# Kernel optimization log

Measured on AMD Instinct MI355X. Metric: run time of the kernel, lower is better.

## Reference

```python
import jax, jax.numpy as jnp
import numpy as np

# static config (mirrors init_kwargs)
B, IMG_C, IN_C, OUT_C, S = 16, 3, 256, 512, 128
HIDDEN = IN_C                     # min(out_dim, in_dim) in DepthwiseSynthesisKernel
KGEN_IN = 32                      # (3+1)//2 * 4 * (512//128)
KSIZE = 3                         # generated depthwise kernel taps (= conv_kernel)
NUM_TAPS = KGEN_IN - 2 * KSIZE + 2  # 28, low-pass filter taps
CUTOFF, HALFWIDTH = 32.0, 7.35
CONV_CLAMP = 256.0
LRELU_GAIN = float(np.sqrt(2.0))  # bias_act def_gain for lrelu
DN = ('NCHW', 'OIHW', 'NCHW')

def _firwin(numtaps, cutoff, width, fs):
    # numpy re-implementation of scipy.signal.firwin (kaiser window, lowpass)
    nyq = fs / 2.0
    atten = 2.285 * (numtaps - 1) * np.pi * (width / nyq) + 7.95
    if atten > 50:
        beta = 0.1102 * (atten - 8.7)
    elif atten > 21:
        beta = 0.5842 * (atten - 21) ** 0.4 + 0.07886 * (atten - 21)
    else:
        beta = 0.0
    m = np.arange(numtaps) - (numtaps - 1) / 2.0
    c = cutoff / nyq
    h = c * np.sinc(c * m) * np.kaiser(numtaps, beta)
    return (h / h.sum()).astype(np.float32)

def setup_inputs():
    key = jax.random.key(0)
    ks = jax.random.split(key, 9)
    img = jax.random.normal(ks[0], (B, IMG_C, S, S), jnp.float32)
    fromrgb_w = jax.random.normal(ks[1], (IN_C, IMG_C, 1, 1), jnp.float32)
    fromrgb_b = jnp.zeros((IN_C,), jnp.float32)
    freqs = jax.random.normal(ks[2], (HIDDEN, 2), jnp.float32)
    radii = jnp.sqrt(jnp.sum(freqs ** 2, axis=1, keepdims=True))
    freqs = freqs / (radii * jnp.exp(radii ** 2) ** 0.25) * 8.0  # w0_init = 8
    phases = jax.random.uniform(ks[3], (HIDDEN,), jnp.float32) - 0.5
    hz_outdim = jax.random.normal(ks[4], (IN_C, HIDDEN), jnp.float32)
    vt_outdim = jax.random.normal(ks[5], (IN_C, HIDDEN), jnp.float32)
    gauss_sigma = jnp.ones((), jnp.float32)
    lr_weight0 = jax.random.normal(ks[6], (IN_C, IN_C, 1, 1), jnp.float32) / np.sqrt(IN_C)
    point_w = jax.random.normal(ks[7], (OUT_C, IN_C, 1, 1), jnp.float32)
    point_b = jnp.zeros((OUT_C,), jnp.float32)
    low_filter = jnp.asarray(_firwin(NUM_TAPS, CUTOFF, HALFWIDTH * 2, CUTOFF * 2 ** 1.1))
    gauss_x = jnp.arange(KGEN_IN, dtype=jnp.float32) - (KGEN_IN - 1) / 2.0
    fir = jnp.array([1.0, 3.0, 3.0, 1.0], jnp.float32)
    fir = fir / fir.sum()  # upfirdn2d.setup_filter normalization
    return dict(img=img, fromrgb_w=fromrgb_w, fromrgb_b=fromrgb_b, freqs=freqs,
                phases=phases, hz_outdim=hz_outdim, vt_outdim=vt_outdim,
                gauss_sigma=gauss_sigma, lr_weight0=lr_weight0, point_w=point_w,
                point_b=point_b, low_filter=low_filter, gauss_x=gauss_x, fir=fir)

def _conv(x, w, stride=(1, 1), pad=((0, 0), (0, 0)), groups=1):
    return jax.lax.conv_general_dilated(x, w, stride, pad,
                                        feature_group_count=groups,
                                        dimension_numbers=DN)

def _bias_act(x, b, act, gain, clamp):
    x = x + b[None, :, None, None]
    if act == 'lrelu':
        x = jnp.where(x >= 0, x, 0.2 * x)
    x = x * gain
    return jnp.clip(x, -clamp, clamp)

def _sample_weight(grid, coeff, gauss_sigma, gauss_x, low_filter):
    # grid: [HIDDEN, KGEN_IN], coeff: [IN_C, HIDDEN] -> [IN_C, KSIZE]
    basis = jnp.sin(grid * (2.0 * jnp.pi)) * np.float32(np.exp(-0.5))  # density = 1
    w = jnp.einsum('cg,ic->ig', basis, coeff) / np.float32(np.sqrt(HIDDEN))
    w = w - w.mean()
    w = w * jax.lax.rsqrt(jnp.mean(w * w, axis=0, keepdims=True) + 1e-8)
    gs = 1.0 + gauss_sigma ** 2 / 5.0
    w = w * jnp.exp(-(gauss_x ** 2) / (2.0 * gs))
    # valid 1D correlation with low-pass filter, then stride-2 pick
    w = jax.lax.conv_general_dilated(w[:, None, :], low_filter[None, None, :], (1,),
                                     [(0, 0)], dimension_numbers=('NCH', 'OIH', 'NCH'))[:, 0, :]
    return w[:, ::2]

def _forward(img, fromrgb_w, fromrgb_b, freqs, phases, hz_outdim, vt_outdim,
             gauss_sigma, lr_weight0, point_w, point_b, low_filter, gauss_x, fir):
    # fromrgb: Conv2dLayer(act='linear') applies sin() to input, then conv + bias + clamp
    x = jnp.sin(img)
    x = _conv(x, fromrgb_w * np.float32(1.0 / np.sqrt(IMG_C)))  # weight_gain 1/sqrt(in*k^2)
    x = _bias_act(x, fromrgb_b, 'linear', 1.0, CONV_CLAMP)
    # conv0_gen: generate separable depthwise kernels
    g = (jnp.arange(KGEN_IN, dtype=jnp.float32) - (KGEN_IN - 1) / 2.0) * (2.0 / (KGEN_IN + 1))
    hz = _sample_weight(freqs[:, 0:1] * g[None, :] + phases[:, None], hz_outdim,
                        gauss_sigma, gauss_x, low_filter)  # [IN_C, 3]
    vt = _sample_weight(freqs[:, 1:2] * g[None, :] + phases[:, None], vt_outdim,
                        gauss_sigma, gauss_x, low_filter)
    gdw = np.float32(1.0 / np.sqrt(KSIZE))  # Conv2dWrapper weight_gain, I=1, kHkW=3
    y = _conv(x, (vt * gdw).reshape(IN_C, 1, KSIZE, 1), pad=((1, 1), (0, 0)), groups=IN_C)
    y = _conv(y, (hz * gdw).reshape(IN_C, 1, 1, KSIZE), pad=((0, 0), (1, 1)), groups=IN_C)
    # low-rank 1x1 residual path (lr_weight0 via Conv2dWrapper: extra 1/sqrt(IN_C) gain)
    y = y + _conv(x, lr_weight0 * np.float32(1.0 / np.sqrt(IN_C)))
    # conv0_point: 1x1, lrelu, gain sqrt(2), clamp
    y = _conv(y, point_w * np.float32(1.0 / np.sqrt(IN_C)))
    y = _bias_act(y, point_b, 'lrelu', LRELU_GAIN, CONV_CLAMP)
    # FIR downsample by 2 with separable [1,3,3,1]/8 filter (upfirdn2d.downsample2d)
    fv = jnp.broadcast_to(fir.reshape(1, 1, 4, 1), (OUT_C, 1, 4, 1))
    fh = jnp.broadcast_to(fir.reshape(1, 1, 1, 4), (OUT_C, 1, 1, 4))
    y = _conv(y, fv, stride=(2, 1), pad=((1, 1), (0, 0)), groups=OUT_C)
    y = _conv(y, fh, stride=(1, 2), pad=((0, 0), (1, 1)), groups=OUT_C)
    return y  # [B, OUT_C, S//2, S//2]

def reference(img, fromrgb_w, fromrgb_b, freqs, phases, hz_outdim, vt_outdim,
              gauss_sigma, lr_weight0, point_w, point_b, low_filter, gauss_x, fir):
    return _forward(img, fromrgb_w, fromrgb_b, freqs, phases, hz_outdim, vt_outdim,
                    gauss_sigma, lr_weight0, point_w, point_b, low_filter, gauss_x, fir)
```

## Files before the change

kernel.cpp:

```cpp
#include <hip/hip_runtime.h>

typedef __attribute__((ext_vector_type(4))) float f32x4;
typedef __attribute__((ext_vector_type(8))) short s16x8;
typedef unsigned short u16;

#define KGEN 32
#define NTAPS 28

__device__ __forceinline__ float bf2f(u16 v) {
    return __uint_as_float(((unsigned)v) << 16);
}
__device__ __forceinline__ u16 f2bf(float f) {
    unsigned u = __float_as_uint(f);
    unsigned r = (u + 0x7fffu + ((u >> 16) & 1u)) >> 16;
    return (u16)r;
}

#define ASYNC_COPY16(gptr, lptr)                                               \
    __builtin_amdgcn_global_load_lds(                                          \
        (const __attribute__((address_space(1))) unsigned int*)(gptr),         \
        (__attribute__((address_space(3))) unsigned int*)(lptr), 16, 0, 0)

__global__ __launch_bounds__(256) void gen_kernel(
    const float* __restrict__ freqs, const float* __restrict__ phases,
    const float* __restrict__ hz_outdim, const float* __restrict__ vt_outdim,
    const float* __restrict__ gsig, const float* __restrict__ low_filter,
    const float* __restrict__ gauss_x, float* __restrict__ hzvt)
{
    const int which = blockIdx.x;
    const int i = threadIdx.x;

    __shared__ float basis[256][KGEN];
    __shared__ float red[256];
    __shared__ float colscale[KGEN];

    {
        float f = freqs[i * 2 + which];
        float p = phases[i];
        #pragma unroll
        for (int j = 0; j < KGEN; j++) {
            float g = ((float)j - 15.5f) * (2.0f / 33.0f);
            basis[i][j] = sinf((f * g + p) * 6.283185307179586f) * 0.6065306597126334f;
        }
    }
    __syncthreads();

    const float* coeff = (which == 0) ? hz_outdim : vt_outdim;
    float acc[KGEN];
    #pragma unroll
    for (int j = 0; j < KGEN; j++) acc[j] = 0.f;

    const float4* crow = (const float4*)(coeff + (size_t)i * 256);
    for (int c4 = 0; c4 < 64; c4++) {
        float4 cv = crow[c4];
        int c = c4 * 4;
        #pragma unroll
        for (int j = 0; j < KGEN; j++) {
            acc[j] += basis[c][j] * cv.x + basis[c + 1][j] * cv.y
                    + basis[c + 2][j] * cv.z + basis[c + 3][j] * cv.w;
        }
    }
    #pragma unroll
    for (int j = 0; j < KGEN; j++) acc[j] *= 0.0625f;

    float s = 0.f;
    #pragma unroll
    for (int j = 0; j < KGEN; j++) s += acc[j];
    red[i] = s;
    __syncthreads();
    for (int st = 128; st > 0; st >>= 1) {
        if (i < st) red[i] += red[i + st];
        __syncthreads();
    }
    float mean = red[0] * (1.0f / 8192.0f);
    #pragma unroll
    for (int j = 0; j < KGEN; j++) acc[j] -= mean;

    #pragma unroll
    for (int j = 0; j < KGEN; j++) basis[i][j] = acc[j];
    __syncthreads();
    if (i < KGEN) {
        float ss = 0.f;
        for (int r = 0; r < 256; r++) { float v = basis[r][i]; ss += v * v; }
        colscale[i] = rsqrtf(ss * (1.0f / 256.0f) + 1e-8f);
    }
    __syncthreads();

    float sg = gsig[0];
    float gs = 1.0f + sg * sg * 0.2f;
    #pragma unroll
    for (int j = 0; j < KGEN; j++) {
        float gx = gauss_x[j];
        acc[j] = acc[j] * colscale[j] * expf(-(gx * gx) / (2.0f * gs));
    }

    float lf[NTAPS];
    #pragma unroll
    for (int t = 0; t < NTAPS; t++) lf[t] = low_filter[t];
    #pragma unroll
    for (int p = 0; p < 3; p++) {
        int t0 = 2 * p;
        float o = 0.f;
        #pragma unroll
        for (int t = 0; t < NTAPS; t++) o += acc[t0 + t] * lf[t];
        hzvt[((size_t)which * 256 + i) * 3 + p] = o;
    }
}

__global__ __launch_bounds__(256) void fold_kernel(
    const float* __restrict__ point_w, const float* __restrict__ lr_w,
    u16* __restrict__ wcat)
{
    const int n = blockIdx.x;
    const int j = threadIdx.x;
    __shared__ float pw[256];
    pw[j] = point_w[(size_t)n * 256 + j];
    __syncthreads();
    float a0 = 0.f, a1 = 0.f, a2 = 0.f, a3 = 0.f;
    for (int c = 0; c < 256; c += 4) {
        a0 += pw[c + 0] * lr_w[(size_t)(c + 0) * 256 + j];
        a1 += pw[c + 1] * lr_w[(size_t)(c + 1) * 256 + j];
        a2 += pw[c + 2] * lr_w[(size_t)(c + 2) * 256 + j];
        a3 += pw[c + 3] * lr_w[(size_t)(c + 3) * 256 + j];
    }
    float acc = (a0 + a1) + (a2 + a3);
    wcat[(size_t)n * 512 + j]       = f2bf(pw[j] * 0.0625f);
    wcat[(size_t)n * 512 + 256 + j] = f2bf(acc * (1.0f / 256.0f));
}

__global__ __launch_bounds__(256) void fromrgb_kernel(
    const float* __restrict__ img, const float* __restrict__ frw,
    const float* __restrict__ frb, u16* __restrict__ xu)
{
    const int t = threadIdx.x;
    const int pos = blockIdx.x * 8 + (t >> 5);
    const int c0 = (t & 31) * 8;
    const int b = pos >> 14;
    const int hw = pos & 16383;

    const float* ib = img + (size_t)b * 3 * 16384 + hw;
    float s0 = sinf(ib[0]);
    float s1 = sinf(ib[16384]);
    float s2 = sinf(ib[32768]);
    const float g = 0.5773502691896258f;

    union { float4 v[6]; float f[24]; } wv;
    const float4* wp = (const float4*)(frw + (size_t)c0 * 3);
    #pragma unroll
    for (int q = 0; q < 6; q++) wv.v[q] = wp[q];

    union { u16 q[8]; s16x8 v; } ov;
    #pragma unroll
    for (int q = 0; q < 8; q++) {
        float v = (s0 * wv.f[q * 3 + 0] + s1 * wv.f[q * 3 + 1] + s2 * wv.f[q * 3 + 2]) * g
                + frb[c0 + q];
        v = fminf(256.f, fmaxf(-256.f, v));
        ov.q[q] = f2bf(v);
    }
    *(s16x8*)(xu + (size_t)pos * 512 + 256 + c0) = ov.v;
}

__global__ __launch_bounds__(256) void dw_kernel(
    u16* __restrict__ xu, const float* __restrict__ hzvt)
{
    const int t = blockIdx.x * 256 + threadIdx.x;
    const int c0 = (t & 31) * 8;
    const int pos = t >> 5;
    const int w = pos & 127;
    const int h = (pos >> 7) & 127;
    const int b = pos >> 14;

    union { float4 v[6]; float f[24]; } hzw, vtw;
    const float4* hp = (const float4*)(hzvt + (size_t)c0 * 3);
    const float4* vp = (const float4*)(hzvt + 768 + (size_t)c0 * 3);
    #pragma unroll
    for (int q = 0; q < 6; q++) { hzw.v[q] = hp[q]; vtw.v[q] = vp[q]; }

    float acc8[8];
    #pragma unroll
    for (int q = 0; q < 8; q++) acc8[q] = 0.f;

    #pragma unroll
    for (int i = 0; i < 3; i++) {
        int hh = h + i - 1;
        if (hh < 0 || hh > 127) continue;
        float hr[8];
        #pragma unroll
        for (int q = 0; q < 8; q++) hr[q] = 0.f;
        #pragma unroll
        for (int j = 0; j < 3; j++) {
            int ww = w + j - 1;
            if (ww < 0 || ww > 127) continue;
            const u16* xp = xu + ((size_t)((b * 128 + hh) * 128 + ww) * 512 + 256 + c0);
            s16x8 xv = *(const s16x8*)xp;
            #pragma unroll
            for (int q = 0; q < 8; q++) hr[q] += hzw.f[q * 3 + j] * bf2f((u16)xv[q]);
        }
        #pragma unroll
        for (int q = 0; q < 8; q++) acc8[q] += vtw.f[q * 3 + i] * hr[q];
    }

    union { u16 q[8]; s16x8 v; } ov;
    #pragma unroll
    for (int q = 0; q < 8; q++) ov.q[q] = f2bf(acc8[q] * (1.0f / 3.0f));
    *(s16x8*)(xu + (size_t)pos * 512 + c0) = ov.v;
}

__global__ __launch_bounds__(256) void gemm_kernel(
    const u16* __restrict__ xu, const u16* __restrict__ wcat,
    const float* __restrict__ point_b, u16* __restrict__ ypre, int nofs)
{
    __shared__ u16 As[128 * 32];
    __shared__ u16 Bs[128 * 32];

    const int tid = threadIdx.x;
    const int bid = blockIdx.x;
    const int ntile = (bid >> 3) & 1;
    const int mtile = (bid & 7) | ((bid >> 4) << 3);

    const int erow = tid >> 2;
    const int ek = tid & 3;
    const size_t apos0 = (size_t)(mtile * 128 + erow) * 512 + ek * 8;
    const size_t apos1 = apos0 + (size_t)64 * 512;
    const int nbase = nofs + ntile * 128;
    const size_t bpos0 = (size_t)(nbase + erow) * 512 + ek * 8;
    const size_t bpos1 = bpos0 + (size_t)64 * 512;
    u16* as0 = &As[(size_t)tid * 8];
    u16* as1 = &As[(size_t)(tid + 256) * 8];
    u16* bs0 = &Bs[(size_t)tid * 8];
    u16* bs1 = &Bs[(size_t)(tid + 256) * 8];

    const int lane = tid & 63;
    const int wave = tid >> 6;
    const int wm = (wave >> 1) * 64;
    const int wn = (wave & 1) * 64;
    const int l16 = lane & 15;
    const int lq = lane >> 4;

    f32x4 acc[4][4];
    #pragma unroll
    for (int a = 0; a < 4; a++)
        #pragma unroll
        for (int c = 0; c < 4; c++) acc[a][c] = (f32x4){0.f, 0.f, 0.f, 0.f};

    for (int kt = 0; kt < 16; kt++) {
        __syncthreads();
        const int ko = kt * 32;
        ASYNC_COPY16(xu + apos0 + ko, as0);
        ASYNC_COPY16(xu + apos1 + ko, as1);
        ASYNC_COPY16(wcat + bpos0 + ko, bs0);
        ASYNC_COPY16(wcat + bpos1 + ko, bs1);
        __syncthreads();

        s16x8 af[4], bf[4];
        #pragma unroll
        for (int mi = 0; mi < 4; mi++)
            af[mi] = *(const s16x8*)&As[(wm + mi * 16 + l16) * 32 + lq * 8];
        #pragma unroll
        for (int ni = 0; ni < 4; ni++)
            bf[ni] = *(const s16x8*)&Bs[(wn + ni * 16 + l16) * 32 + lq * 8];
        #pragma unroll
        for (int mi = 0; mi < 4; mi++)
            #pragma unroll
            for (int ni = 0; ni < 4; ni++)
                acc[mi][ni] = __builtin_amdgcn_mfma_f32_16x16x32_bf16(
                    af[mi], bf[ni], acc[mi][ni], 0, 0, 0);
    }

    const int b = mtile >> 7;
    const int h = mtile & 127;
    #pragma unroll
    for (int ni = 0; ni < 4; ni++) {
        const int nl = ntile * 128 + wn + ni * 16 + l16;
        const float bias = point_b[nofs + nl];
        u16* drow = ypre + ((size_t)(b * 256 + nl) * 128 + h) * 128;
        #pragma unroll
        for (int mi = 0; mi < 4; mi++) {
            const int w0 = wm + mi * 16 + lq * 4;
            union { u16 q[4]; uint2 d; } pk;
            #pragma unroll
            for (int r = 0; r < 4; r++) {
                float v = acc[mi][ni][r] + bias;
                v = (v >= 0.f) ? v : 0.2f * v;
                v *= 1.4142135623730951f;
                v = fminf(256.f, fmaxf(-256.f, v));
                pk.q[r] = f2bf(v);
            }
            *(uint2*)(drow + w0) = pk.d;
        }
    }
}

__global__ __launch_bounds__(64) void fir_kernel(
    const u16* __restrict__ ypre, const float* __restrict__ fir,
    float* __restrict__ out, int nofs)
{
    const int bid = blockIdx.x;
    const int lane = threadIdx.x;
    const int nl = bid & 255;
    const int b = bid >> 8;
    const u16* src = ypre + (size_t)(b * 256 + nl) * 16384;
    float* dst = out + (size_t)(b * 512 + nofs + nl) * 4096;

    const float f0 = fir[0], f1 = fir[1], f2 = fir[2], f3 = fir[3];

    auto hrow = [&](int r) -> float {
        if (r < 0 || r > 127) return 0.f;
        unsigned raw = *(const unsigned*)(src + (size_t)r * 128 + lane * 2);
        float y0 = bf2f((u16)(raw & 0xffffu));
        float y1 = bf2f((u16)(raw >> 16));
        float ym = __shfl_up(y1, 1u);
        if (lane == 0) ym = 0.f;
        float yp = __shfl_down(y0, 1u);
        if (lane == 63) yp = 0.f;
        return f0 * ym + f1 * y0 + f2 * y1 + f3 * yp;
    };

    float A = 0.f;
    float Bv = hrow(0);
    for (int oh = 0; oh < 64; oh++) {
        float C = hrow(2 * oh + 1);
        float D = hrow(2 * oh + 2);
        dst[oh * 64 + lane] = f0 * A + f1 * Bv + f2 * C + f3 * D;
        A = C;
        Bv = D;
    }
}

extern "C" void kernel_launch(void* const* d_in, const int* in_sizes, int n_in,
                              void* d_out, int out_size, void* d_ws, size_t ws_size,
                              hipStream_t stream)
{
    (void)in_sizes; (void)n_in; (void)out_size; (void)ws_size;
    const float* img        = (const float*)d_in[0];
    const float* fromrgb_w  = (const float*)d_in[1];
    const float* fromrgb_b  = (const float*)d_in[2];
    const float* freqs      = (const float*)d_in[3];
    const float* phases     = (const float*)d_in[4];
    const float* hz_outdim  = (const float*)d_in[5];
    const float* vt_outdim  = (const float*)d_in[6];
    const float* gsig       = (const float*)d_in[7];
    const float* lr_w       = (const float*)d_in[8];
    const float* point_w    = (const float*)d_in[9];
    const float* point_b    = (const float*)d_in[10];
    const float* low_filter = (const float*)d_in[11];
    const float* gauss_x    = (const float*)d_in[12];
    const float* fir        = (const float*)d_in[13];

    char* ws = (char*)d_ws;
    u16*   xu   = (u16*)(ws);
    u16*   ypre = (u16*)(ws + 268435456LL);
    u16*   wcat = (u16*)(ws + 402653184LL);
    float* hzvt = (float*)(ws + 403177472LL);
    float* out  = (float*)d_out;

    hipLaunchKernelGGL(gen_kernel, dim3(2), dim3(256), 0, stream,
                       freqs, phases, hz_outdim, vt_outdim, gsig, low_filter, gauss_x, hzvt);
    hipLaunchKernelGGL(fold_kernel, dim3(512), dim3(256), 0, stream,
                       point_w, lr_w, wcat);
    hipLaunchKernelGGL(fromrgb_kernel, dim3(32768), dim3(256), 0, stream,
                       img, fromrgb_w, fromrgb_b, xu);
    hipLaunchKernelGGL(dw_kernel, dim3(32768), dim3(256), 0, stream,
                       xu, hzvt);
    for (int half = 0; half < 2; half++) {
        hipLaunchKernelGGL(gemm_kernel, dim3(4096), dim3(256), 0, stream,
                           xu, wcat, point_b, ypre, half * 256);
        hipLaunchKernelGGL(fir_kernel, dim3(4096), dim3(64), 0, stream,
                           ypre, fir, out, half * 256);
    }
}
```

Measured before the change: 746.3 us.

## Merge prep kernels, deepen GEMM K-tile with swizzled LDS, split FIR rows across waves

Three independent changes. The three setup kernels (filter generation, weight folding, fromrgb) become one launch that dispatches on block index, removing launch gaps. The GEMM now stages 64-wide K tiles instead of 32 and uses an XOR swizzle on the LDS layout, which halves the barrier count and is meant to cut bank conflicts. The FIR kernel uses four waves per block, each producing 16 output rows, to raise occupancy at the cost of reloading a couple of overlap rows. The merged prep kernel reserves the gen kernel's large shared-memory footprint for every block, which may lower occupancy for the fromrgb blocks.

```diff
diff --git a/kernel.cpp b/kernel.cpp
--- a/kernel.cpp
+++ b/kernel.cpp
@@ -21,143 +21,144 @@
         (const __attribute__((address_space(1))) unsigned int*)(gptr),         \
         (__attribute__((address_space(3))) unsigned int*)(lptr), 16, 0, 0)
 
-__global__ __launch_bounds__(256) void gen_kernel(
+__global__ __launch_bounds__(256) void prep_kernel(
     const float* __restrict__ freqs, const float* __restrict__ phases,
     const float* __restrict__ hz_outdim, const float* __restrict__ vt_outdim,
     const float* __restrict__ gsig, const float* __restrict__ low_filter,
-    const float* __restrict__ gauss_x, float* __restrict__ hzvt)
-{
-    const int which = blockIdx.x;
-    const int i = threadIdx.x;
-
-    __shared__ float basis[256][KGEN];
-    __shared__ float red[256];
-    __shared__ float colscale[KGEN];
-
-    {
-        float f = freqs[i * 2 + which];
-        float p = phases[i];
-        #pragma unroll
-        for (int j = 0; j < KGEN; j++) {
-            float g = ((float)j - 15.5f) * (2.0f / 33.0f);
-            basis[i][j] = sinf((f * g + p) * 6.283185307179586f) * 0.6065306597126334f;
-        }
-    }
-    __syncthreads();
-
-    const float* coeff = (which == 0) ? hz_outdim : vt_outdim;
-    float acc[KGEN];
-    #pragma unroll
-    for (int j = 0; j < KGEN; j++) acc[j] = 0.f;
-
-    const float4* crow = (const float4*)(coeff + (size_t)i * 256);
-    for (int c4 = 0; c4 < 64; c4++) {
-        float4 cv = crow[c4];
-        int c = c4 * 4;
-        #pragma unroll
-        for (int j = 0; j < KGEN; j++) {
-            acc[j] += basis[c][j] * cv.x + basis[c + 1][j] * cv.y
-                    + basis[c + 2][j] * cv.z + basis[c + 3][j] * cv.w;
-        }
-    }
-    #pragma unroll
-    for (int j = 0; j < KGEN; j++) acc[j] *= 0.0625f;
-
-    float s = 0.f;
-    #pragma unroll
-    for (int j = 0; j < KGEN; j++) s += acc[j];
-    red[i] = s;
-    __syncthreads();
-    for (int st = 128; st > 0; st >>= 1) {
-        if (i < st) red[i] += red[i + st];
-        __syncthreads();
-    }
-    float mean = red[0] * (1.0f / 8192.0f);
-    #pragma unroll
-    for (int j = 0; j < KGEN; j++) acc[j] -= mean;
-
-    #pragma unroll
-    for (int j = 0; j < KGEN; j++) basis[i][j] = acc[j];
-    __syncthreads();
-    if (i < KGEN) {
-        float ss = 0.f;
-        for (int r = 0; r < 256; r++) { float v = basis[r][i]; ss += v * v; }
-        colscale[i] = rsqrtf(ss * (1.0f / 256.0f) + 1e-8f);
-    }
-    __syncthreads();
-
-    float sg = gsig[0];
-    float gs = 1.0f + sg * sg * 0.2f;
-    #pragma unroll
-    for (int j = 0; j < KGEN; j++) {
-        float gx = gauss_x[j];
-        acc[j] = acc[j] * colscale[j] * expf(-(gx * gx) / (2.0f * gs));
-    }
-
-    float lf[NTAPS];
-    #pragma unroll
-    for (int t = 0; t < NTAPS; t++) lf[t] = low_filter[t];
-    #pragma unroll
-    for (int p = 0; p < 3; p++) {
-        int t0 = 2 * p;
-        float o = 0.f;
-        #pragma unroll
-        for (int t = 0; t < NTAPS; t++) o += acc[t0 + t] * lf[t];
-        hzvt[((size_t)which * 256 + i) * 3 + p] = o;
-    }
-}
-
-__global__ __launch_bounds__(256) void fold_kernel(
+    const float* __restrict__ gauss_x, float* __restrict__ hzvt,
     const float* __restrict__ point_w, const float* __restrict__ lr_w,
-    u16* __restrict__ wcat)
-{
-    const int n = blockIdx.x;
-    const int j = threadIdx.x;
-    __shared__ float pw[256];
-    pw[j] = point_w[(size_t)n * 256 + j];
-    __syncthreads();
-    float a0 = 0.f, a1 = 0.f, a2 = 0.f, a3 = 0.f;
-    for (int c = 0; c < 256; c += 4) {
-        a0 += pw[c + 0] * lr_w[(size_t)(c + 0) * 256 + j];
-        a1 += pw[c + 1] * lr_w[(size_t)(c + 1) * 256 + j];
-        a2 += pw[c + 2] * lr_w[(size_t)(c + 2) * 256 + j];
-        a3 += pw[c + 3] * lr_w[(size_t)(c + 3) * 256 + j];
-    }
-    float acc = (a0 + a1) + (a2 + a3);
-    wcat[(size_t)n * 512 + j]       = f2bf(pw[j] * 0.0625f);
-    wcat[(size_t)n * 512 + 256 + j] = f2bf(acc * (1.0f / 256.0f));
-}
-
-__global__ __launch_bounds__(256) void fromrgb_kernel(
+    u16* __restrict__ wcat,
     const float* __restrict__ img, const float* __restrict__ frw,
     const float* __restrict__ frb, u16* __restrict__ xu)
 {
+    __shared__ union {
+        struct {
+            float basis[256][KGEN];
+            float red[256];
+            float colscale[KGEN];
+        } g;
+        float pw[256];
+    } sm;
+
+    const int bidx = blockIdx.x;
     const int t = threadIdx.x;
-    const int pos = blockIdx.x * 8 + (t >> 5);
-    const int c0 = (t & 31) * 8;
-    const int b = pos >> 14;
-    const int hw = pos & 16383;
-
-    const float* ib = img + (size_t)b * 3 * 16384 + hw;
-    float s0 = sinf(ib[0]);
-    float s1 = sinf(ib[16384]);
-    float s2 = sinf(ib[32768]);
-    const float g = 0.5773502691896258f;
-
-    union { float4 v[6]; float f[24]; } wv;
-    const float4* wp = (const float4*)(frw + (size_t)c0 * 3);
-    #pragma unroll
-    for (int q = 0; q < 6; q++) wv.v[q] = wp[q];
-
-    union { u16 q[8]; s16x8 v; } ov;
-    #pragma unroll
-    for (int q = 0; q < 8; q++) {
-        float v = (s0 * wv.f[q * 3 + 0] + s1 * wv.f[q * 3 + 1] + s2 * wv.f[q * 3 + 2]) * g
-                + frb[c0 + q];
-        v = fminf(256.f, fmaxf(-256.f, v));
-        ov.q[q] = f2bf(v);
-    }
-    *(s16x8*)(xu + (size_t)pos * 512 + 256 + c0) = ov.v;
+
+    if (bidx < 2) {
+        const int which = bidx;
+        const int i = t;
+        {
+            float f = freqs[i * 2 + which];
+            float p = phases[i];
+            #pragma unroll
+            for (int j = 0; j < KGEN; j++) {
+                float g = ((float)j - 15.5f) * (2.0f / 33.0f);
+                sm.g.basis[i][j] = sinf((f * g + p) * 6.283185307179586f) * 0.6065306597126334f;
+            }
+        }
+        __syncthreads();
+
+        const float* coeff = (which == 0) ? hz_outdim : vt_outdim;
+        float acc[KGEN];
+        #pragma unroll
+        for (int j = 0; j < KGEN; j++) acc[j] = 0.f;
+
+        const float4* crow = (const float4*)(coeff + (size_t)i * 256);
+        for (int c4 = 0; c4 < 64; c4++) {
+            float4 cv = crow[c4];
+            int c = c4 * 4;
+            #pragma unroll
+            for (int j = 0; j < KGEN; j++) {
+                acc[j] += sm.g.basis[c][j] * cv.x + sm.g.basis[c + 1][j] * cv.y
+                        + sm.g.basis[c + 2][j] * cv.z + sm.g.basis[c + 3][j] * cv.w;
+            }
+        }
+        #pragma unroll
+        for (int j = 0; j < KGEN; j++) acc[j] *= 0.0625f;
+
+        float s = 0.f;
+        #pragma unroll
+        for (int j = 0; j < KGEN; j++) s += acc[j];
+        sm.g.red[i] = s;
+        __syncthreads();
+        for (int st = 128; st > 0; st >>= 1) {
+            if (i < st) sm.g.red[i] += sm.g.red[i + st];
+            __syncthreads();
+        }
+        float mean = sm.g.red[0] * (1.0f / 8192.0f);
+        #pragma unroll
+        for (int j = 0; j < KGEN; j++) acc[j] -= mean;
+
+        #pragma unroll
+        for (int j = 0; j < KGEN; j++) sm.g.basis[i][j] = acc[j];
+        __syncthreads();
+        if (i < KGEN) {
+            float ss = 0.f;
+            for (int r = 0; r < 256; r++) { float v = sm.g.basis[r][i]; ss += v * v; }
+            sm.g.colscale[i] = rsqrtf(ss * (1.0f / 256.0f) + 1e-8f);
+        }
+        __syncthreads();
+
+        float sg = gsig[0];
+        float gs = 1.0f + sg * sg * 0.2f;
+        #pragma unroll
+        for (int j = 0; j < KGEN; j++) {
+            float gx = gauss_x[j];
+            acc[j] = acc[j] * sm.g.colscale[j] * expf(-(gx * gx) / (2.0f * gs));
+        }
+
+        float lf[NTAPS];
+        #pragma unroll
+        for (int tt = 0; tt < NTAPS; tt++) lf[tt] = low_filter[tt];
+        #pragma unroll
+        for (int p = 0; p < 3; p++) {
+            int t0 = 2 * p;
+            float o = 0.f;
+            #pragma unroll
+            for (int tt = 0; tt < NTAPS; tt++) o += acc[t0 + tt] * lf[tt];
+            hzvt[((size_t)which * 256 + i) * 3 + p] = o;
+        }
+    } else if (bidx < 514) {
+        const int n = bidx - 2;
+        const int j = t;
+        sm.pw[j] = point_w[(size_t)n * 256 + j];
+        __syncthreads();
+        float a0 = 0.f, a1 = 0.f, a2 = 0.f, a3 = 0.f;
+        for (int c = 0; c < 256; c += 4) {
+            a0 += sm.pw[c + 0] * lr_w[(size_t)(c + 0) * 256 + j];
+            a1 += sm.pw[c + 1] * lr_w[(size_t)(c + 1) * 256 + j];
+            a2 += sm.pw[c + 2] * lr_w[(size_t)(c + 2) * 256 + j];
+            a3 += sm.pw[c + 3] * lr_w[(size_t)(c + 3) * 256 + j];
+        }
+        float acc = (a0 + a1) + (a2 + a3);
+        wcat[(size_t)n * 512 + j]       = f2bf(sm.pw[j] * 0.0625f);
+        wcat[(size_t)n * 512 + 256 + j] = f2bf(acc * (1.0f / 256.0f));
+    } else {
+        const int pos = (bidx - 514) * 8 + (t >> 5);
+        const int c0 = (t & 31) * 8;
+        const int b = pos >> 14;
+        const int hw = pos & 16383;
+
+        const float* ib = img + (size_t)b * 3 * 16384 + hw;
+        float s0 = sinf(ib[0]);
+        float s1 = sinf(ib[16384]);
+        float s2 = sinf(ib[32768]);
+        const float g = 0.5773502691896258f;
+
+        union { float4 v[6]; float f[24]; } wv;
+        const float4* wp = (const float4*)(frw + (size_t)c0 * 3);
+        #pragma unroll
+        for (int q = 0; q < 6; q++) wv.v[q] = wp[q];
+
+        union { u16 q[8]; s16x8 v; } ov;
+        #pragma unroll
+        for (int q = 0; q < 8; q++) {
+            float v = (s0 * wv.f[q * 3 + 0] + s1 * wv.f[q * 3 + 1] + s2 * wv.f[q * 3 + 2]) * g
+                    + frb[c0 + q];
+            v = fminf(256.f, fmaxf(-256.f, v));
+            ov.q[q] = f2bf(v);
+        }
+        *(s16x8*)(xu + (size_t)pos * 512 + 256 + c0) = ov.v;
+    }
 }
 
 __global__ __launch_bounds__(256) void dw_kernel(
@@ -210,25 +211,22 @@
     const u16* __restrict__ xu, const u16* __restrict__ wcat,
     const float* __restrict__ point_b, u16* __restrict__ ypre, int nofs)
 {
-    __shared__ u16 As[128 * 32];
-    __shared__ u16 Bs[128 * 32];
+    __shared__ u16 As[128 * 64];
+    __shared__ u16 Bs[128 * 64];
 
     const int tid = threadIdx.x;
     const int bid = blockIdx.x;
     const int ntile = (bid >> 3) & 1;
     const int mtile = (bid & 7) | ((bid >> 4) << 3);
 
-    const int erow = tid >> 2;
-    const int ek = tid & 3;
-    const size_t apos0 = (size_t)(mtile * 128 + erow) * 512 + ek * 8;
-    const size_t apos1 = apos0 + (size_t)64 * 512;
+    const int srow = tid >> 3;
+    const int slot = tid & 7;
+    const int ek = slot ^ (srow & 7);
+    const size_t abase = (size_t)(mtile * 128 + srow) * 512 + ek * 8;
     const int nbase = nofs + ntile * 128;
-    const size_t bpos0 = (size_t)(nbase + erow) * 512 + ek * 8;
-    const size_t bpos1 = bpos0 + (size_t)64 * 512;
-    u16* as0 = &As[(size_t)tid * 8];
-    u16* as1 = &As[(size_t)(tid + 256) * 8];
-    u16* bs0 = &Bs[(size_t)tid * 8];
-    u16* bs1 = &Bs[(size_t)(tid + 256) * 8];
+    const size_t bbase = (size_t)(nbase + srow) * 512 + ek * 8;
+    u16* asdst = &As[(size_t)tid * 8];
+    u16* bsdst = &Bs[(size_t)tid * 8];
 
     const int lane = tid & 63;
     const int wave = tid >> 6;
@@ -243,28 +241,36 @@
         #pragma unroll
         for (int c = 0; c < 4; c++) acc[a][c] = (f32x4){0.f, 0.f, 0.f, 0.f};
 
-    for (int kt = 0; kt < 16; kt++) {
-        __syncthreads();
-        const int ko = kt * 32;
-        ASYNC_COPY16(xu + apos0 + ko, as0);
-        ASYNC_COPY16(xu + apos1 + ko, as1);
-        ASYNC_COPY16(wcat + bpos0 + ko, bs0);
-        ASYNC_COPY16(wcat + bpos1 + ko, bs1);
-        __syncthreads();
-
-        s16x8 af[4], bf[4];
-        #pragma unroll
-        for (int mi = 0; mi < 4; mi++)
-            af[mi] = *(const s16x8*)&As[(wm + mi * 16 + l16) * 32 + lq * 8];
-        #pragma unroll
-        for (int ni = 0; ni < 4; ni++)
-            bf[ni] = *(const s16x8*)&Bs[(wn + ni * 16 + l16) * 32 + lq * 8];
-        #pragma unroll
-        for (int mi = 0; mi < 4; mi++)
-            #pragma unroll
-            for (int ni = 0; ni < 4; ni++)
-                acc[mi][ni] = __builtin_amdgcn_mfma_f32_16x16x32_bf16(
-                    af[mi], bf[ni], acc[mi][ni], 0, 0, 0);
+    for (int kt = 0; kt < 8; kt++) {
+        __syncthreads();
+        const int ko = kt * 64;
+        #pragma unroll
+        for (int i = 0; i < 4; i++) {
+            ASYNC_COPY16(xu + abase + (size_t)i * 32 * 512 + ko, asdst + i * 2048);
+            ASYNC_COPY16(wcat + bbase + (size_t)i * 32 * 512 + ko, bsdst + i * 2048);
+        }
+        __syncthreads();
+
+        #pragma unroll
+        for (int kk = 0; kk < 2; kk++) {
+            s16x8 af[4], bf[4];
+            #pragma unroll
+            for (int mi = 0; mi < 4; mi++) {
+                const int r = wm + mi * 16 + l16;
+                af[mi] = *(const s16x8*)&As[r * 64 + (((kk * 4 + lq) ^ (r & 7)) * 8)];
+            }
+            #pragma unroll
+            for (int ni = 0; ni < 4; ni++) {
+                const int r = wn + ni * 16 + l16;
+                bf[ni] = *(const s16x8*)&Bs[r * 64 + (((kk * 4 + lq) ^ (r & 7)) * 8)];
+            }
+            #pragma unroll
+            for (int mi = 0; mi < 4; mi++)
+                #pragma unroll
+                for (int ni = 0; ni < 4; ni++)
+                    acc[mi][ni] = __builtin_amdgcn_mfma_f32_16x16x32_bf16(
+                        af[mi], bf[ni], acc[mi][ni], 0, 0, 0);
+        }
     }
 
     const int b = mtile >> 7;
@@ -291,12 +297,14 @@
     }
 }
 
-__global__ __launch_bounds__(64) void fir_kernel(
+__global__ __launch_bounds__(256) void fir_kernel(
     const u16* __restrict__ ypre, const float* __restrict__ fir,
     float* __restrict__ out, int nofs)
 {
     const int bid = blockIdx.x;
-    const int lane = threadIdx.x;
+    const int tid = threadIdx.x;
+    const int lane = tid & 63;
+    const int wave = tid >> 6;
     const int nl = bid & 255;
     const int b = bid >> 8;
     const u16* src = ypre + (size_t)(b * 256 + nl) * 16384;
@@ -316,9 +324,10 @@
         return f0 * ym + f1 * y0 + f2 * y1 + f3 * yp;
     };
 
-    float A = 0.f;
-    float Bv = hrow(0);
-    for (int oh = 0; oh < 64; oh++) {
+    const int oh0 = wave * 16;
+    float A = hrow(2 * oh0 - 1);
+    float Bv = hrow(2 * oh0);
+    for (int oh = oh0; oh < oh0 + 16; oh++) {
         float C = hrow(2 * oh + 1);
         float D = hrow(2 * oh + 2);
         dst[oh * 64 + lane] = f0 * A + f1 * Bv + f2 * C + f3 * D;
@@ -354,18 +363,15 @@
     float* hzvt = (float*)(ws + 403177472LL);
     float* out  = (float*)d_out;
 
-    hipLaunchKernelGGL(gen_kernel, dim3(2), dim3(256), 0, stream,
-                       freqs, phases, hz_outdim, vt_outdim, gsig, low_filter, gauss_x, hzvt);
-    hipLaunchKernelGGL(fold_kernel, dim3(512), dim3(256), 0, stream,
-                       point_w, lr_w, wcat);
-    hipLaunchKernelGGL(fromrgb_kernel, dim3(32768), dim3(256), 0, stream,
-                       img, fromrgb_w, fromrgb_b, xu);
+    hipLaunchKernelGGL(prep_kernel, dim3(33282), dim3(256), 0, stream,
+                       freqs, phases, hz_outdim, vt_outdim, gsig, low_filter, gauss_x, hzvt,
+                       point_w, lr_w, wcat, img, fromrgb_w, fromrgb_b, xu);
     hipLaunchKernelGGL(dw_kernel, dim3(32768), dim3(256), 0, stream,
                        xu, hzvt);
     for (int half = 0; half < 2; half++) {
         hipLaunchKernelGGL(gemm_kernel, dim3(4096), dim3(256), 0, stream,
                            xu, wcat, point_b, ypre, half * 256);
-        hipLaunchKernelGGL(fir_kernel, dim3(4096), dim3(64), 0, stream,
+        hipLaunchKernelGGL(fir_kernel, dim3(4096), dim3(256), 0, stream,
                            ypre, fir, out, half * 256);
     }
 }
```

New measurement: 747.0 us. No clear change (+0.1%).
